# Performance work log

Measured on AMD Instinct MI355X. Metric: run time of the kernel, lower is better.

Reference implementation:

```python
import jax, jax.numpy as jnp
import numpy as np

EPS = 1e-5

def layer_norm(x, g, b):
    mu = jnp.mean(x, axis=-1, keepdims=True)
    var = jnp.var(x, axis=-1, keepdims=True)
    return (x - mu) * jax.lax.rsqrt(var + EPS) * g + b

def setup_inputs() -> dict:
    key = jax.random.key(0)
    ks = jax.random.split(key, 8)
    B, N, C, H = 4, 1024, 1024, 16
    Dh = C * 4
    std = 0.02
    return {
        "x": jax.random.normal(ks[0], (B, N, C), dtype=jnp.float32),
        "qkv_w": jax.random.normal(ks[1], (3 * C, C), dtype=jnp.float32) * std,
        "proj_w": jax.random.normal(ks[2], (C, C), dtype=jnp.float32) * std,
        "proj_b": jnp.zeros((C,), dtype=jnp.float32),
        "fc1_w": jax.random.normal(ks[3], (Dh, C), dtype=jnp.float32) * std,
        "fc1_b": jnp.zeros((Dh,), dtype=jnp.float32),
        "fc2_w": jax.random.normal(ks[4], (C, Dh), dtype=jnp.float32) * std,
        "fc2_b": jnp.zeros((C,), dtype=jnp.float32),
        "ln1_g": jnp.ones((C,), dtype=jnp.float32),
        "ln1_b": jnp.zeros((C,), dtype=jnp.float32),
        "ln2_g": jnp.ones((C,), dtype=jnp.float32),
        "ln2_b": jnp.zeros((C,), dtype=jnp.float32),
        "lnh_g": jnp.ones((Dh,), dtype=jnp.float32),
        "lnh_b": jnp.zeros((Dh,), dtype=jnp.float32),
    }

def reference(x, qkv_w, proj_w, proj_b, fc1_w, fc1_b, fc2_w, fc2_b,
              ln1_g, ln1_b, ln2_g, ln2_b, lnh_g, lnh_b):
    B, N, C = x.shape
    H = 16
    Dh = C // H
    scale = Dh ** (-0.5)

    # --- attention sublayer (pre-norm) ---
    h = layer_norm(x, ln1_g, ln1_b)
    qkv = (h @ qkv_w.T).reshape(B, N, 3, H, Dh).transpose(2, 0, 3, 1, 4)  # [3,B,H,N,Dh]
    q, k, v = qkv[0], qkv[1], qkv[2]
    attn = jnp.einsum('bhid,bhjd->bhij', q, k) * scale
    attn = jax.nn.softmax(attn, axis=-1)
    o = jnp.einsum('bhij,bhjd->bhid', attn, v)          # [B,H,N,Dh]
    o = o.transpose(0, 2, 1, 3).reshape(B, N, C)
    o = o @ proj_w.T + proj_b
    x = x + o

    # --- MLP sublayer (pre-norm, with LN on hidden per use_ln=True) ---
    h = layer_norm(x, ln2_g, ln2_b)
    u = jax.nn.gelu(h @ fc1_w.T + fc1_b, approximate=False)  # torch nn.GELU = erf form
    u = layer_norm(u, lnh_g, lnh_b)
    m = u @ fc2_w.T + fc2_b
    return x + m
```

## Files before the change

kernel.cpp:

```cpp
#include <hip/hip_runtime.h>
#include <hip/hip_bf16.h>
#include <math.h>


#define TOKENS 4096
#define CDIM   1024
#define HEADS  16
#define DHEAD  64
#define HID    4096

typedef __attribute__((ext_vector_type(4))) float  floatx4;
typedef __attribute__((ext_vector_type(8))) short  short8;

__global__ __launch_bounds__(256) void cvt_all(
    const float* __restrict__ s0, const float* __restrict__ s1,
    const float* __restrict__ s2, const float* __restrict__ s3,
    __hip_bfloat16* __restrict__ dst)
{
    long i = (long)blockIdx.x * 256 + threadIdx.x;
    const float* src;
    long base;
    if (i < 768l * 1024)       { src = s0; base = 0; }
    else if (i < 1792l * 1024) { src = s1; base = 768l * 1024; }
    else if (i < 2816l * 1024) { src = s2; base = 1792l * 1024; }
    else                       { src = s3; base = 2816l * 1024; }
    float4 v = ((const float4*)src)[i - base];
    __hip_bfloat16 t[4];
    t[0] = __float2bfloat16(v.x);
    t[1] = __float2bfloat16(v.y);
    t[2] = __float2bfloat16(v.z);
    t[3] = __float2bfloat16(v.w);
    *(uint2*)(dst + 4l * i) = *(uint2*)t;
}

__global__ __launch_bounds__(256) void ln_f32_kernel(
    const float* __restrict__ x, const float* __restrict__ g,
    const float* __restrict__ b, __hip_bfloat16* __restrict__ y, int C)
{
    int row = blockIdx.x;
    const float* xr = x + (long)row * C;
    __hip_bfloat16* yr = y + (long)row * C;

    float s = 0.f, ss = 0.f;
    for (int i = threadIdx.x; i < C; i += 256) {
        float v = xr[i];
        s += v; ss += v * v;
    }
    #pragma unroll
    for (int d = 32; d; d >>= 1) {
        s  += __shfl_down(s, d);
        ss += __shfl_down(ss, d);
    }
    __shared__ float buf[4][2];
    int wid = threadIdx.x >> 6, lane = threadIdx.x & 63;
    if (lane == 0) { buf[wid][0] = s; buf[wid][1] = ss; }
    __syncthreads();
    if (threadIdx.x == 0) {
        s = buf[0][0] + buf[1][0] + buf[2][0] + buf[3][0];
        ss = buf[0][1] + buf[1][1] + buf[2][1] + buf[3][1];
        buf[0][0] = s; buf[0][1] = ss;
    }
    __syncthreads();
    s = buf[0][0]; ss = buf[0][1];

    float invC = 1.f / (float)C;
    float mu = s * invC;
    float var = ss * invC - mu * mu;
    float inv = rsqrtf(var + 1e-5f);
    for (int i = threadIdx.x; i < C; i += 256) {
        yr[i] = __float2bfloat16((xr[i] - mu) * inv * g[i] + b[i]);
    }
}

__global__ __launch_bounds__(256) void ln_bf16_kernel(
    const __hip_bfloat16* __restrict__ x, const float* __restrict__ g,
    const float* __restrict__ b, __hip_bfloat16* __restrict__ y, int C)
{
    int row = blockIdx.x;
    const __hip_bfloat16* xr = x + (long)row * C;
    __hip_bfloat16* yr = y + (long)row * C;

    float s = 0.f, ss = 0.f;
    for (int i = threadIdx.x; i < C; i += 256) {
        float v = __bfloat162float(xr[i]);
        s += v; ss += v * v;
    }
    #pragma unroll
    for (int d = 32; d; d >>= 1) {
        s  += __shfl_down(s, d);
        ss += __shfl_down(ss, d);
    }
    __shared__ float buf[4][2];
    int wid = threadIdx.x >> 6, lane = threadIdx.x & 63;
    if (lane == 0) { buf[wid][0] = s; buf[wid][1] = ss; }
    __syncthreads();
    if (threadIdx.x == 0) {
        s = buf[0][0] + buf[1][0] + buf[2][0] + buf[3][0];
        ss = buf[0][1] + buf[1][1] + buf[2][1] + buf[3][1];
        buf[0][0] = s; buf[0][1] = ss;
    }
    __syncthreads();
    s = buf[0][0]; ss = buf[0][1];

    float invC = 1.f / (float)C;
    float mu = s * invC;
    float var = ss * invC - mu * mu;
    float inv = rsqrtf(var + 1e-5f);
    for (int i = threadIdx.x; i < C; i += 256) {
        float v = __bfloat162float(xr[i]);
        yr[i] = __float2bfloat16((v - mu) * inv * g[i] + b[i]);
    }
}

template <int TN>
__global__ __launch_bounds__(256, 3) void gemm_mfma(
    const __hip_bfloat16* __restrict__ A,
    const __hip_bfloat16* __restrict__ W,
    const float* __restrict__ bias, const float* __restrict__ residual,
    void* __restrict__ Cout, int M, int N, int K, int act, int out_bf16)
{
    constexpr int WN = (TN == 128) ? 2 : 1;
    constexpr int WM = 4 / WN;
    constexpr int FJ = 4;
    constexpr int FI = 128 / (WM * 16);

    __shared__ __hip_bfloat16 Asl[2][128 * 32];
    __shared__ __hip_bfloat16 Bsl[2][TN * 32];

    int tid = threadIdx.x;
    int wave = tid >> 6, lane = tid & 63;
    int bm = blockIdx.y * 128, bn = blockIdx.x * TN;
    int wm = wave & (WM - 1), wn = wave / WM;
    int fm = lane & 15, quad = lane >> 4;

    int srow = lane >> 2;
    int skk  = (lane & 3) * 8;

    const __hip_bfloat16* Ap = A + (long)(bm + wave * 16 + srow) * K + skk;
    const __hip_bfloat16* Bp = W + (long)(bn + wave * 16 + srow) * K + skk;
    const long a64 = (long)64 * K;

    const int nk = K / 32;
    floatx4 acc[FI][FJ] = {};
    const int aoff = (wave * 16 + srow) * 32 + skk;

    uint4 a0 = *(const uint4*)(Ap);
    uint4 a1 = *(const uint4*)(Ap + a64);
    uint4 b0 = *(const uint4*)(Bp);
    uint4 b1 = {};
    if (TN == 128) b1 = *(const uint4*)(Bp + a64);

    *(uint4*)&Asl[0][aoff] = a0;
    *(uint4*)&Asl[0][aoff + 2048] = a1;
    *(uint4*)&Bsl[0][aoff] = b0;
    if (TN == 128) *(uint4*)&Bsl[0][aoff + 2048] = b1;

    a0 = *(const uint4*)(Ap + 32);
    a1 = *(const uint4*)(Ap + a64 + 32);
    b0 = *(const uint4*)(Bp + 32);
    if (TN == 128) b1 = *(const uint4*)(Bp + a64 + 32);

    __syncthreads();

    for (int kt = 0; kt < nk; ++kt) {
        const int buf = kt & 1;
        const __hip_bfloat16* Ab = Asl[buf];
        const __hip_bfloat16* Bb = Bsl[buf];

        short8 bfr[FJ];
        #pragma unroll
        for (int j = 0; j < FJ; ++j)
            bfr[j] = *(const short8*)(Bb + (wn * 64 + j * 16 + fm) * 32 + quad * 8);
        #pragma unroll
        for (int i = 0; i < FI; ++i) {
            short8 af = *(const short8*)(Ab + (wm * FI * 16 + i * 16 + fm) * 32 + quad * 8);
            #pragma unroll
            for (int j = 0; j < FJ; ++j)
                acc[i][j] = __builtin_amdgcn_mfma_f32_16x16x32_bf16(
                    af, bfr[j], acc[i][j], 0, 0, 0);
        }

        if (kt + 1 < nk) {
            const int nb = buf ^ 1;
            *(uint4*)&Asl[nb][aoff] = a0;
            *(uint4*)&Asl[nb][aoff + 2048] = a1;
            *(uint4*)&Bsl[nb][aoff] = b0;
            if (TN == 128) *(uint4*)&Bsl[nb][aoff + 2048] = b1;
            if (kt + 2 < nk) {
                const long o = (long)(kt + 2) * 32;
                a0 = *(const uint4*)(Ap + o);
                a1 = *(const uint4*)(Ap + a64 + o);
                b0 = *(const uint4*)(Bp + o);
                if (TN == 128) b1 = *(const uint4*)(Bp + a64 + o);
            }
        }
        __syncthreads();
    }

    int mbase = bm + wm * FI * 16;
    int nbase = bn + wn * 64;
    #pragma unroll
    for (int i = 0; i < FI; ++i) {
        #pragma unroll
        for (int j = 0; j < FJ; ++j) {
            int ncol = nbase + j * 16 + fm;
            #pragma unroll
            for (int r = 0; r < 4; ++r) {
                int mrow = mbase + i * 16 + quad * 4 + r;
                float v = acc[i][j][r];
                if (bias) v += bias[ncol];
                if (act == 1) v = 0.5f * v * (1.f + erff(v * 0.70710678118654752f));
                if (residual) v += residual[(long)mrow * N + ncol];
                if (out_bf16)
                    ((__hip_bfloat16*)Cout)[(long)mrow * N + ncol] = __float2bfloat16(v);
                else
                    ((float*)Cout)[(long)mrow * N + ncol] = v;
            }
        }
    }
}

__global__ __launch_bounds__(256) void attn_mfma(
    const __hip_bfloat16* __restrict__ qkv, __hip_bfloat16* __restrict__ o_out)
{
    __shared__ __align__(16) char Ks[64 * 144];
    __shared__ __align__(16) char Vt[64 * 144];
    __shared__ __align__(16) char Ps[4 * 16 * 144];

    const int C3 = 3 * CDIM;
    int wg = blockIdx.x;
    int bh = wg >> 4, qt = wg & 15;
    int b = bh >> 4, hh = bh & 15;
    int tid = threadIdx.x, wave = tid >> 6, lane = tid & 63;
    int l = lane & 15, quad = lane >> 4;

    const __hip_bfloat16* qrow =
        qkv + (long)(b * 1024 + qt * 64 + wave * 16 + l) * C3 + hh * DHEAD;
    short8 qf0 = *(const short8*)(qrow + quad * 8);
    short8 qf1 = *(const short8*)(qrow + 32 + quad * 8);

    char* Psw = Ps + wave * (16 * 144);

    int sc = tid & 7;
    int skl = tid >> 3;

    const __hip_bfloat16* Kbase = qkv + (long)(b * 1024) * C3 + CDIM + hh * DHEAD;
    const __hip_bfloat16* Vbase = qkv + (long)(b * 1024) * C3 + 2 * CDIM + hh * DHEAD;

    floatx4 facc[4] = {};
    float mrun = -1e30f, lrun = 0.f;

    #pragma unroll 1
    for (int kt = 0; kt < 16; ++kt) {
        __syncthreads();
        {
            const __hip_bfloat16* Kg = Kbase + (long)(kt * 64) * C3;
            #pragma unroll
            for (int it = 0; it < 2; ++it) {
                int key = skl + 32 * it;
                uint4 kv = *(const uint4*)(Kg + (long)key * C3 + sc * 8);
                *(uint4*)(Ks + key * 144 + sc * 16) = kv;
            }
            const __hip_bfloat16* Vg = Vbase + (long)(kt * 64) * C3;
            uint4 v0 = *(const uint4*)(Vg + (long)(2 * skl) * C3 + sc * 8);
            uint4 v1 = *(const uint4*)(Vg + (long)(2 * skl + 1) * C3 + sc * 8);
            const ushort* e0 = (const ushort*)&v0;
            const ushort* e1 = (const ushort*)&v1;
            int kpp = skl ^ (sc << 2);
            #pragma unroll
            for (int j = 0; j < 8; ++j) {
                unsigned dw = (unsigned)e0[j] | ((unsigned)e1[j] << 16);
                int d = sc * 8 + j;
                *(unsigned*)(Vt + d * 144 + kpp * 4) = dw;
            }
        }
        __syncthreads();

        floatx4 st[4] = {};
        #pragma unroll
        for (int kb = 0; kb < 4; ++kb) {
            short8 k0 = *(const short8*)(Ks + (kb * 16 + l) * 144 + quad * 16);
            short8 k1 = *(const short8*)(Ks + (kb * 16 + l) * 144 + 64 + quad * 16);
            st[kb] = __builtin_amdgcn_mfma_f32_16x16x32_bf16(k0, qf0, st[kb], 0, 0, 0);
            st[kb] = __builtin_amdgcn_mfma_f32_16x16x32_bf16(k1, qf1, st[kb], 0, 0, 0);
        }

        float p[16];
        float tm = -1e30f;
        #pragma unroll
        for (int kb = 0; kb < 4; ++kb)
            #pragma unroll
            for (int r = 0; r < 4; ++r) {
                float s = st[kb][r] * 0.125f;
                p[kb * 4 + r] = s;
                tm = fmaxf(tm, s);
            }
        tm = fmaxf(tm, __shfl_xor(tm, 16));
        tm = fmaxf(tm, __shfl_xor(tm, 32));
        float mn = fmaxf(mrun, tm);
        float alpha = __expf(mrun - mn);
        float psum = 0.f;
        #pragma unroll
        for (int i = 0; i < 16; ++i) { p[i] = __expf(p[i] - mn); psum += p[i]; }
        psum += __shfl_xor(psum, 16);
        psum += __shfl_xor(psum, 32);
        lrun = lrun * alpha + psum;
        mrun = mn;

        #pragma unroll
        for (int kb = 0; kb < 4; ++kb) {
            __hip_bfloat16 t[4];
            #pragma unroll
            for (int r = 0; r < 4; ++r) t[r] = __float2bfloat16(p[kb * 4 + r]);
            *(uint2*)(Psw + l * 144 + kb * 32 + quad * 8) = *(const uint2*)t;
        }

        float a0 = __shfl(alpha, quad * 4 + 0);
        float a1 = __shfl(alpha, quad * 4 + 1);
        float a2 = __shfl(alpha, quad * 4 + 2);
        float a3 = __shfl(alpha, quad * 4 + 3);
        #pragma unroll
        for (int db = 0; db < 4; ++db) {
            facc[db][0] *= a0; facc[db][1] *= a1;
            facc[db][2] *= a2; facc[db][3] *= a3;
        }

        short8 pf0 = *(const short8*)(Psw + l * 144 + quad * 16);
        short8 pf1 = *(const short8*)(Psw + l * 144 + 64 + quad * 16);
        #pragma unroll
        for (int db = 0; db < 4; ++db) {
            int d = db * 16 + l;
            int o3 = (d >> 3) & 7;
            short8 v0 = *(const short8*)(Vt + d * 144 + ((quad ^ o3) << 4));
            short8 v1 = *(const short8*)(Vt + d * 144 + (((4 + quad) ^ o3) << 4));
            facc[db] = __builtin_amdgcn_mfma_f32_16x16x32_bf16(pf0, v0, facc[db], 0, 0, 0);
            facc[db] = __builtin_amdgcn_mfma_f32_16x16x32_bf16(pf1, v1, facc[db], 0, 0, 0);
        }
    }

    float il0 = 1.f / __shfl(lrun, quad * 4 + 0);
    float il1 = 1.f / __shfl(lrun, quad * 4 + 1);
    float il2 = 1.f / __shfl(lrun, quad * 4 + 2);
    float il3 = 1.f / __shfl(lrun, quad * 4 + 3);
    __hip_bfloat16* orow =
        o_out + (long)(b * 1024 + qt * 64 + wave * 16) * CDIM + hh * DHEAD;
    #pragma unroll
    for (int db = 0; db < 4; ++db) {
        int col = db * 16 + l;
        orow[(quad * 4 + 0) * CDIM + col] = __float2bfloat16(facc[db][0] * il0);
        orow[(quad * 4 + 1) * CDIM + col] = __float2bfloat16(facc[db][1] * il1);
        orow[(quad * 4 + 2) * CDIM + col] = __float2bfloat16(facc[db][2] * il2);
        orow[(quad * 4 + 3) * CDIM + col] = __float2bfloat16(facc[db][3] * il3);
    }
}

extern "C" void kernel_launch(void* const* d_in, const int* in_sizes, int n_in,
                              void* d_out, int out_size, void* d_ws, size_t ws_size,
                              hipStream_t stream)
{
    const float* x      = (const float*)d_in[0];
    const float* qkv_w  = (const float*)d_in[1];
    const float* proj_w = (const float*)d_in[2];
    const float* proj_b = (const float*)d_in[3];
    const float* fc1_w  = (const float*)d_in[4];
    const float* fc1_b  = (const float*)d_in[5];
    const float* fc2_w  = (const float*)d_in[6];
    const float* fc2_b  = (const float*)d_in[7];
    const float* ln1_g  = (const float*)d_in[8];
    const float* ln1_b  = (const float*)d_in[9];
    const float* ln2_g  = (const float*)d_in[10];
    const float* ln2_b  = (const float*)d_in[11];
    const float* lnh_g  = (const float*)d_in[12];
    const float* lnh_b  = (const float*)d_in[13];

    float* out = (float*)d_out;

    __hip_bfloat16* wsb     = (__hip_bfloat16*)d_ws;
    __hip_bfloat16* qkvw_bf = wsb;
    __hip_bfloat16* fc1w_bf = qkvw_bf + 3l * 1024 * 1024;
    __hip_bfloat16* fc2w_bf = fc1w_bf + 4l * 1024 * 1024;
    __hip_bfloat16* projw_bf= fc2w_bf + 4l * 1024 * 1024;
    __hip_bfloat16* h_bf    = projw_bf + 1l * 1024 * 1024;
    __hip_bfloat16* qkv_bf  = h_bf + 4l * 1024 * 1024;
    __hip_bfloat16* o_bf    = qkv_bf + 12l * 1024 * 1024;
    __hip_bfloat16* u_bf    = o_bf + 4l * 1024 * 1024;

    cvt_all<<<12288, 256, 0, stream>>>(qkv_w, fc1_w, fc2_w, proj_w, qkvw_bf);

    ln_f32_kernel<<<TOKENS, 256, 0, stream>>>(x, ln1_g, ln1_b, h_bf, CDIM);
    gemm_mfma<128><<<dim3(3072 / 128, TOKENS / 128), 256, 0, stream>>>(
        h_bf, qkvw_bf, nullptr, nullptr, qkv_bf, TOKENS, 3072, CDIM, 0, 1);
    attn_mfma<<<1024, 256, 0, stream>>>(qkv_bf, o_bf);
    gemm_mfma<64><<<dim3(CDIM / 64, TOKENS / 128), 256, 0, stream>>>(
        o_bf, projw_bf, proj_b, x, out, TOKENS, CDIM, CDIM, 0, 0);
    ln_f32_kernel<<<TOKENS, 256, 0, stream>>>(out, ln2_g, ln2_b, h_bf, CDIM);
    gemm_mfma<128><<<dim3(HID / 128, TOKENS / 128), 256, 0, stream>>>(
        h_bf, fc1w_bf, fc1_b, nullptr, u_bf, TOKENS, HID, CDIM, 1, 1);
    ln_bf16_kernel<<<TOKENS, 256, 0, stream>>>(u_bf, lnh_g, lnh_b, u_bf, HID);
    gemm_mfma<64><<<dim3(CDIM / 64, TOKENS / 128), 256, 0, stream>>>(
        u_bf, fc2w_bf, fc2_b, out, out, TOKENS, CDIM, HID, 0, 0);
}
```

Measured before the change: 410.6 us.

## Deepen GEMM/attention load pipelining and remap blocks for XCD L2 locality

The GEMM main loop is unrolled by two and keeps two register sets of global prefetch, so tiles are loaded two k-steps ahead of the MFMA work. The attention kernel gets double-buffered K and V tiles in shared memory, with the next tile's global load issued before the current tile's compute. Both kernels also remap linear block IDs so that blocks landing on the same XCD work on neighbouring M tiles or the same head, to improve L2 reuse. The cost is more live registers for prefetch and twice the attention LDS, which can lower occupancy.

```diff
diff --git a/kernel.cpp b/kernel.cpp
--- a/kernel.cpp
+++ b/kernel.cpp
@@ -129,7 +129,19 @@
 
     int tid = threadIdx.x;
     int wave = tid >> 6, lane = tid & 63;
-    int bm = blockIdx.y * 128, bn = blockIdx.x * TN;
+
+    int mt, nt;
+    {
+        int gx = gridDim.x, gy = gridDim.y;
+        int lin = blockIdx.y * gx + blockIdx.x;
+        if ((gy & 7) == 0) {
+            int chunk = gy >> 3;
+            int xcd = lin & 7, q = lin >> 3;
+            mt = xcd * chunk + (q % chunk);
+            nt = q / chunk;
+        } else { mt = blockIdx.y; nt = blockIdx.x; }
+    }
+    int bm = mt * 128, bn = nt * TN;
     int wm = wave & (WM - 1), wn = wave / WM;
     int fm = lane & 15, quad = lane >> 4;
 
@@ -144,29 +156,23 @@
     floatx4 acc[FI][FJ] = {};
     const int aoff = (wave * 16 + srow) * 32 + skk;
 
-    uint4 a0 = *(const uint4*)(Ap);
-    uint4 a1 = *(const uint4*)(Ap + a64);
-    uint4 b0 = *(const uint4*)(Bp);
-    uint4 b1 = {};
-    if (TN == 128) b1 = *(const uint4*)(Bp + a64);
-
-    *(uint4*)&Asl[0][aoff] = a0;
-    *(uint4*)&Asl[0][aoff + 2048] = a1;
-    *(uint4*)&Bsl[0][aoff] = b0;
-    if (TN == 128) *(uint4*)&Bsl[0][aoff + 2048] = b1;
-
-    a0 = *(const uint4*)(Ap + 32);
-    a1 = *(const uint4*)(Ap + a64 + 32);
-    b0 = *(const uint4*)(Bp + 32);
-    if (TN == 128) b1 = *(const uint4*)(Bp + a64 + 32);
-
-    __syncthreads();
-
-    for (int kt = 0; kt < nk; ++kt) {
-        const int buf = kt & 1;
+    uint4 a0A, a1A, b0A, b1A;
+    uint4 a0B, a1B, b0B, b1B;
+
+#define GLOADA(t) { const long o = (long)(t) * 32; \
+    a0A = *(const uint4*)(Ap + o); a1A = *(const uint4*)(Ap + a64 + o); \
+    b0A = *(const uint4*)(Bp + o); if (TN == 128) b1A = *(const uint4*)(Bp + a64 + o); }
+#define GLOADB(t) { const long o = (long)(t) * 32; \
+    a0B = *(const uint4*)(Ap + o); a1B = *(const uint4*)(Ap + a64 + o); \
+    b0B = *(const uint4*)(Bp + o); if (TN == 128) b1B = *(const uint4*)(Bp + a64 + o); }
+#define LWRITEA(bf) { *(uint4*)&Asl[bf][aoff] = a0A; *(uint4*)&Asl[bf][aoff + 2048] = a1A; \
+    *(uint4*)&Bsl[bf][aoff] = b0A; if (TN == 128) *(uint4*)&Bsl[bf][aoff + 2048] = b1A; }
+#define LWRITEB(bf) { *(uint4*)&Asl[bf][aoff] = a0B; *(uint4*)&Asl[bf][aoff + 2048] = a1B; \
+    *(uint4*)&Bsl[bf][aoff] = b0B; if (TN == 128) *(uint4*)&Bsl[bf][aoff + 2048] = b1B; }
+
+    auto compute = [&](int buf) {
         const __hip_bfloat16* Ab = Asl[buf];
         const __hip_bfloat16* Bb = Bsl[buf];
-
         short8 bfr[FJ];
         #pragma unroll
         for (int j = 0; j < FJ; ++j)
@@ -179,23 +185,29 @@
                 acc[i][j] = __builtin_amdgcn_mfma_f32_16x16x32_bf16(
                     af, bfr[j], acc[i][j], 0, 0, 0);
         }
-
-        if (kt + 1 < nk) {
-            const int nb = buf ^ 1;
-            *(uint4*)&Asl[nb][aoff] = a0;
-            *(uint4*)&Asl[nb][aoff + 2048] = a1;
-            *(uint4*)&Bsl[nb][aoff] = b0;
-            if (TN == 128) *(uint4*)&Bsl[nb][aoff + 2048] = b1;
-            if (kt + 2 < nk) {
-                const long o = (long)(kt + 2) * 32;
-                a0 = *(const uint4*)(Ap + o);
-                a1 = *(const uint4*)(Ap + a64 + o);
-                b0 = *(const uint4*)(Bp + o);
-                if (TN == 128) b1 = *(const uint4*)(Bp + a64 + o);
-            }
-        }
+    };
+
+    GLOADA(0); GLOADB(1);
+    LWRITEA(0);
+    GLOADA(2);
+    __syncthreads();
+
+    for (int kt = 0; kt < nk; kt += 2) {
+        compute(0);
+        LWRITEB(1);
+        if (kt + 3 < nk) GLOADB(kt + 3);
         __syncthreads();
-    }
+        compute(1);
+        if (kt + 2 < nk) {
+            LWRITEA(0);
+            if (kt + 4 < nk) GLOADA(kt + 4);
+        }
+        __syncthreads();
+    }
+#undef GLOADA
+#undef GLOADB
+#undef LWRITEA
+#undef LWRITEB
 
     int mbase = bm + wm * FI * 16;
     int nbase = bn + wn * 64;
@@ -223,13 +235,15 @@
 __global__ __launch_bounds__(256) void attn_mfma(
     const __hip_bfloat16* __restrict__ qkv, __hip_bfloat16* __restrict__ o_out)
 {
-    __shared__ __align__(16) char Ks[64 * 144];
-    __shared__ __align__(16) char Vt[64 * 144];
+    __shared__ __align__(16) char Ks[2][64 * 144];
+    __shared__ __align__(16) char Vt[2][64 * 144];
     __shared__ __align__(16) char Ps[4 * 16 * 144];
 
     const int C3 = 3 * CDIM;
-    int wg = blockIdx.x;
-    int bh = wg >> 4, qt = wg & 15;
+    int lin = blockIdx.x;
+    int xcd = lin & 7, q = lin >> 3;
+    int bh = xcd * 8 + (q >> 4);
+    int qt = q & 15;
     int b = bh >> 4, hh = bh & 15;
     int tid = threadIdx.x, wave = tid >> 6, lane = tid & 63;
     int l = lane & 15, quad = lane >> 4;
@@ -246,45 +260,41 @@
 
     const __hip_bfloat16* Kbase = qkv + (long)(b * 1024) * C3 + CDIM + hh * DHEAD;
     const __hip_bfloat16* Vbase = qkv + (long)(b * 1024) * C3 + 2 * CDIM + hh * DHEAD;
+    const int kpp = skl ^ (sc << 2);
 
     floatx4 facc[4] = {};
     float mrun = -1e30f, lrun = 0.f;
 
-    #pragma unroll 1
-    for (int kt = 0; kt < 16; ++kt) {
-        __syncthreads();
-        {
-            const __hip_bfloat16* Kg = Kbase + (long)(kt * 64) * C3;
-            #pragma unroll
-            for (int it = 0; it < 2; ++it) {
-                int key = skl + 32 * it;
-                uint4 kv = *(const uint4*)(Kg + (long)key * C3 + sc * 8);
-                *(uint4*)(Ks + key * 144 + sc * 16) = kv;
-            }
-            const __hip_bfloat16* Vg = Vbase + (long)(kt * 64) * C3;
-            uint4 v0 = *(const uint4*)(Vg + (long)(2 * skl) * C3 + sc * 8);
-            uint4 v1 = *(const uint4*)(Vg + (long)(2 * skl + 1) * C3 + sc * 8);
-            const ushort* e0 = (const ushort*)&v0;
-            const ushort* e1 = (const ushort*)&v1;
-            int kpp = skl ^ (sc << 2);
-            #pragma unroll
-            for (int j = 0; j < 8; ++j) {
-                unsigned dw = (unsigned)e0[j] | ((unsigned)e1[j] << 16);
-                int d = sc * 8 + j;
-                *(unsigned*)(Vt + d * 144 + kpp * 4) = dw;
-            }
-        }
-        __syncthreads();
-
+    uint4 kA0, kA1, vA0, vA1;
+    uint4 kB0, kB1, vB0, vB1;
+
+#define GKV(t, k0, k1, v0, v1) { \
+    const __hip_bfloat16* Kg = Kbase + (long)((t) * 64) * C3; \
+    const __hip_bfloat16* Vg = Vbase + (long)((t) * 64) * C3; \
+    k0 = *(const uint4*)(Kg + (long)skl * C3 + sc * 8); \
+    k1 = *(const uint4*)(Kg + (long)(skl + 32) * C3 + sc * 8); \
+    v0 = *(const uint4*)(Vg + (long)(2 * skl) * C3 + sc * 8); \
+    v1 = *(const uint4*)(Vg + (long)(2 * skl + 1) * C3 + sc * 8); }
+#define WKV(bf, k0, k1, v0, v1) { \
+    *(uint4*)(Ks[bf] + skl * 144 + sc * 16) = k0; \
+    *(uint4*)(Ks[bf] + (skl + 32) * 144 + sc * 16) = k1; \
+    const ushort* e0 = (const ushort*)&v0; \
+    const ushort* e1 = (const ushort*)&v1; \
+    _Pragma("unroll") \
+    for (int j = 0; j < 8; ++j) { \
+        unsigned dw = (unsigned)e0[j] | ((unsigned)e1[j] << 16); \
+        *(unsigned*)(Vt[bf] + (sc * 8 + j) * 144 + kpp * 4) = dw; \
+    } }
+
+    auto compute = [&](int buf) {
         floatx4 st[4] = {};
         #pragma unroll
         for (int kb = 0; kb < 4; ++kb) {
-            short8 k0 = *(const short8*)(Ks + (kb * 16 + l) * 144 + quad * 16);
-            short8 k1 = *(const short8*)(Ks + (kb * 16 + l) * 144 + 64 + quad * 16);
+            short8 k0 = *(const short8*)(Ks[buf] + (kb * 16 + l) * 144 + quad * 16);
+            short8 k1 = *(const short8*)(Ks[buf] + (kb * 16 + l) * 144 + 64 + quad * 16);
             st[kb] = __builtin_amdgcn_mfma_f32_16x16x32_bf16(k0, qf0, st[kb], 0, 0, 0);
             st[kb] = __builtin_amdgcn_mfma_f32_16x16x32_bf16(k1, qf1, st[kb], 0, 0, 0);
         }
-
         float p[16];
         float tm = -1e30f;
         #pragma unroll
@@ -331,12 +341,27 @@
         for (int db = 0; db < 4; ++db) {
             int d = db * 16 + l;
             int o3 = (d >> 3) & 7;
-            short8 v0 = *(const short8*)(Vt + d * 144 + ((quad ^ o3) << 4));
-            short8 v1 = *(const short8*)(Vt + d * 144 + (((4 + quad) ^ o3) << 4));
+            short8 v0 = *(const short8*)(Vt[buf] + d * 144 + ((quad ^ o3) << 4));
+            short8 v1 = *(const short8*)(Vt[buf] + d * 144 + (((4 + quad) ^ o3) << 4));
             facc[db] = __builtin_amdgcn_mfma_f32_16x16x32_bf16(pf0, v0, facc[db], 0, 0, 0);
             facc[db] = __builtin_amdgcn_mfma_f32_16x16x32_bf16(pf1, v1, facc[db], 0, 0, 0);
         }
-    }
+    };
+
+    GKV(0, kA0, kA1, vA0, vA1);
+    #pragma unroll 1
+    for (int kt = 0; kt < 16; kt += 2) {
+        WKV(0, kA0, kA1, vA0, vA1);
+        __syncthreads();
+        GKV(kt + 1, kB0, kB1, vB0, vB1);
+        compute(0);
+        WKV(1, kB0, kB1, vB0, vB1);
+        __syncthreads();
+        if (kt + 2 < 16) GKV(kt + 2, kA0, kA1, vA0, vA1);
+        compute(1);
+    }
+#undef GKV
+#undef WKV
 
     float il0 = 1.f / __shfl(lrun, quad * 4 + 0);
     float il1 = 1.f / __shfl(lrun, quad * 4 + 1);
```

After: 420.0 us. +2.3%, slower.
